# Kernel tuning notes

Measured on AMD Instinct MI355X. Metric: run time of the kernel, lower is better.

## Reference

```python
import jax, jax.numpy as jnp
import numpy as np

G = 200          # voxel grid extent per axis (spatial_shape)
EPS = 1e-5       # BatchNorm eps


def setup_inputs() -> dict:
    N, C_in, C_out = 1_000_000, 6, 32
    rng = np.random.default_rng(0)
    # unique active voxel sites (submanifold conv assumes deduplicated coords)
    lin = rng.choice(G ** 3, size=N, replace=False)
    coords = np.stack([lin // (G * G), (lin // G) % G, lin % G], axis=1).astype(np.int32)
    key = jax.random.key(0)
    k1, k2 = jax.random.split(key)
    feat = jax.random.normal(k1, (N, C_in), jnp.float32)
    W = jax.random.normal(k2, (27, C_in, C_out), jnp.float32) * (1.0 / np.sqrt(27 * C_in))
    gamma = jnp.ones((C_out,), jnp.float32)
    beta = jnp.zeros((C_out,), jnp.float32)
    return {"feat": feat, "coords": jnp.asarray(coords), "W": W, "gamma": gamma, "beta": beta}


def _subm_conv_bn_relu(feat, coords, W, gamma, beta):
    # Submanifold 3x3x3 sparse conv: output only at active sites.
    N = feat.shape[0]
    c = coords
    keys = (c[:, 0] * G + c[:, 1]) * G + c[:, 2]          # linearized voxel keys
    order = jnp.argsort(keys)
    skeys = keys[order]
    sfeat = feat[order]
    # all 27 kernel offsets, center included
    r = jnp.arange(-1, 2, dtype=c.dtype)
    offs = jnp.stack(jnp.meshgrid(r, r, r, indexing="ij"), -1).reshape(27, 3)

    def step(acc, xs):
        off, Wk = xs                                       # off: [3], Wk: [C_in, C_out]
        nc = c + off                                       # neighbor coords [N,3]
        valid = jnp.all((nc >= 0) & (nc < G), axis=1)
        nkey = (nc[:, 0] * G + nc[:, 1]) * G + nc[:, 2]
        pos = jnp.clip(jnp.searchsorted(skeys, nkey), 0, N - 1)
        found = valid & (skeys[pos] == nkey)               # rulebook hit mask
        g = jnp.where(found[:, None], sfeat[pos], 0.0)     # gathered neighbor feats [N,C_in]
        return acc + g @ Wk, None

    out, _ = jax.lax.scan(step, jnp.zeros((N, W.shape[2]), feat.dtype), (offs, W))
    # BatchNorm1d (training-mode batch stats) + ReLU
    mean = out.mean(0)
    var = out.var(0)
    out = (out - mean) * jax.lax.rsqrt(var + EPS) * gamma + beta
    return jax.nn.relu(out)


def reference(feat, coords, W, gamma, beta):
    return _subm_conv_bn_relu(feat, coords, W, gamma, beta)
```

## Files before the change

### kernel.cpp

```cpp
#include <hip/hip_runtime.h>
#include <stdint.h>

#define GRIDX 200
#define P 202
#define PCELL (P * P * P)
#define GUARD 100000
#define NBITS (PCELL + GUARD)
#define NWP ((NBITS + 31) / 32)
#define K_INV (PCELL + 50000)
#define CIN 6
#define COUT 32
#define NOFF 27
#define BN_EPS 1e-5f
#define WPB 1024
#define NBLKP ((NWP + WPB - 1) / WPB)

typedef __attribute__((ext_vector_type(8))) short short8;
typedef __attribute__((ext_vector_type(4))) float f32x4;


__device__ __forceinline__ int xcd_swizzle(int b, int nwg) {
    int q = nwg >> 3, r = nwg & 7;
    int xcd = b & 7, idx = b >> 3;
    int base = (xcd < r) ? xcd * (q + 1) : r * (q + 1) + (xcd - r) * q;
    return base + idx;
}

__device__ __forceinline__ unsigned short f2bf(float f) {
    uint32_t u = __float_as_uint(f);
    return (unsigned short)((u + 0x7FFFu + ((u >> 16) & 1u)) >> 16);
}
__device__ __forceinline__ uint32_t pack2(float a, float b) {
    return (uint32_t)f2bf(a) | ((uint32_t)f2bf(b) << 16);
}

__device__ __forceinline__ int koff_delta(int koff) {
    int t9 = koff / 9;
    int r9 = koff - t9 * 9;
    int t3 = r9 / 3;
    return (t9 - 1) * (P * P) + (t3 - 1) * P + (r9 - t3 * 3 - 1);
}


__global__ __launch_bounds__(256)
void build_bitmap_v4(const int* __restrict__ coords, int N, uint2* __restrict__ recs) {
    int t = blockIdx.x * blockDim.x + threadIdx.x;
    int i0 = t * 4;
    if (i0 >= N) return;
    if (i0 + 4 <= N) {
        const int4* c4 = (const int4*)(coords + (size_t)i0 * 3);
        int4 ca = c4[0], cb = c4[1], cc = c4[2];
        int cx[4] = {ca.x, ca.w, cb.z, cc.y};
        int cy[4] = {ca.y, cb.x, cb.w, cc.z};
        int cz[4] = {ca.z, cb.y, cc.x, cc.w};
#pragma unroll
        for (int s = 0; s < 4; s++) {
            int key = ((cx[s] + 1) * P + (cy[s] + 1)) * P + (cz[s] + 1);
            atomicOr((unsigned int*)&recs[key >> 5], 1u << (key & 31));
        }
    } else {
        for (int i = i0; i < N; i++) {
            int x = coords[3 * i], y = coords[3 * i + 1], z = coords[3 * i + 2];
            int key = ((x + 1) * P + (y + 1)) * P + (z + 1);
            atomicOr((unsigned int*)&recs[key >> 5], 1u << (key & 31));
        }
    }
}

__global__ __launch_bounds__(256)
void bitmap_count_p(const uint2* __restrict__ recs, int* __restrict__ bcnt) {
    __shared__ int tot[256];
    int b = blockIdx.x, t = threadIdx.x;
    int w0 = b * WPB + t * 4;
    int s = 0;
#pragma unroll
    for (int j = 0; j < 4; j++) {
        int w = w0 + j;
        if (w < NWP) s += __popc(recs[w].x);
    }
    tot[t] = s;
    __syncthreads();
    if (t < 128) tot[t] += tot[t + 128];
    __syncthreads();
    if (t < 64) {
        int v = tot[t] + tot[t + 64];
#pragma unroll
        for (int d = 32; d > 0; d >>= 1) v += __shfl_down(v, d);
        if (t == 0) bcnt[b] = v;
    }
}

__global__ void scan_small(const int* __restrict__ cnt, int* __restrict__ base, int n) {
    __shared__ int tot[256];
    int t = threadIdx.x;
    int v = (t < n) ? cnt[t] : 0;
    tot[t] = v;
    __syncthreads();
    for (int d = 1; d < 256; d <<= 1) {
        int u = (t >= d) ? tot[t - d] : 0;
        __syncthreads();
        tot[t] += u;
        __syncthreads();
    }
    if (t < n) base[t] = tot[t] - v;
}

__global__ __launch_bounds__(256)
void base_fill_skeys(uint2* __restrict__ recs, const int* __restrict__ bbase,
                     int* __restrict__ skeys) {
    __shared__ int tot[256];
    int b = blockIdx.x, t = threadIdx.x;
    int w0 = b * WPB + t * 4;
    uint32_t wd[4];
    int p[4];
    int s = 0;
#pragma unroll
    for (int j = 0; j < 4; j++) {
        int w = w0 + j;
        wd[j] = (w < NWP) ? recs[w].x : 0u;
        p[j] = __popc(wd[j]);
        s += p[j];
    }
    tot[t] = s;
    __syncthreads();
    for (int d = 1; d < 256; d <<= 1) {
        int u = (t >= d) ? tot[t - d] : 0;
        __syncthreads();
        tot[t] += u;
        __syncthreads();
    }
    int run = bbase[b] + tot[t] - s;
#pragma unroll
    for (int j = 0; j < 4; j++) {
        int w = w0 + j;
        if (w < NWP) {
            recs[w].y = (uint32_t)run;
            uint32_t m = wd[j];
            int rr = run;
            int k0 = w * 32;
            while (m) {
                int bit = __ffs((int)m) - 1;
                skeys[rr++] = k0 + bit;
                m &= m - 1u;
            }
            run += p[j];
        }
    }
}


__global__ __launch_bounds__(256)
void rank_scatter_v4(const int* __restrict__ coords, const float* __restrict__ feat, int N,
                     const uint2* __restrict__ recs,
                     int* __restrict__ sorig, uint4* __restrict__ feat_bf) {
    int t = blockIdx.x * blockDim.x + threadIdx.x;
    int i0 = t * 4;
    if (i0 >= N) return;
    if (i0 + 4 <= N) {
        const int4* c4 = (const int4*)(coords + (size_t)i0 * 3);
        int4 ca = c4[0], cb = c4[1], cc = c4[2];
        int cx[4] = {ca.x, ca.w, cb.z, cc.y};
        int cy[4] = {ca.y, cb.x, cb.w, cc.z};
        int cz[4] = {ca.z, cb.y, cc.x, cc.w};
        const float4* f4 = (const float4*)(feat + (size_t)i0 * 6);
        float4 fa = f4[0], fb = f4[1], fc = f4[2], fd = f4[3], fe = f4[4], ff = f4[5];
        float fs[4][6] = {
            {fa.x, fa.y, fa.z, fa.w, fb.x, fb.y},
            {fb.z, fb.w, fc.x, fc.y, fc.z, fc.w},
            {fd.x, fd.y, fd.z, fd.w, fe.x, fe.y},
            {fe.z, fe.w, ff.x, ff.y, ff.z, ff.w}};
#pragma unroll
        for (int s = 0; s < 4; s++) {
            int key = ((cx[s] + 1) * P + (cy[s] + 1)) * P + (cz[s] + 1);
            uint2 rb = recs[key >> 5];
            int bit = key & 31;
            int r = (int)(rb.y + (uint32_t)__popc(rb.x & ((1u << bit) - 1u)));
            sorig[r] = i0 + s;
            uint4 u;
            u.x = pack2(fs[s][0], fs[s][1]);
            u.y = pack2(fs[s][2], fs[s][3]);
            u.z = pack2(fs[s][4], fs[s][5]);
            u.w = 0u;
            feat_bf[r] = u;
        }
    } else {
        for (int i = i0; i < N; i++) {
            int x = coords[3 * i], y = coords[3 * i + 1], z = coords[3 * i + 2];
            int key = ((x + 1) * P + (y + 1)) * P + (z + 1);
            uint2 rb = recs[key >> 5];
            int bit = key & 31;
            int r = (int)(rb.y + (uint32_t)__popc(rb.x & ((1u << bit) - 1u)));
            sorig[r] = i;
            const float* fr = feat + (size_t)i * CIN;
            uint4 u;
            u.x = pack2(fr[0], fr[1]);
            u.y = pack2(fr[2], fr[3]);
            u.z = pack2(fr[4], fr[5]);
            u.w = 0u;
            feat_bf[r] = u;
        }
    }
}


__global__ void prep_wfrag(const float* __restrict__ W, uint4* __restrict__ wfrag) {
    int idx = blockIdx.x * blockDim.x + threadIdx.x;
    if (idx >= 7 * 2 * 64) return;
    int l = idx & 63;
    int nt = (idx >> 6) & 1;
    int ks = idx >> 7;
    int koff = (l >> 4) * 7 + ks;
    int col = nt * 16 + (l & 15);
    unsigned short v[8];
#pragma unroll
    for (int ci = 0; ci < 8; ci++) {
        float f = 0.f;
        if (ci < CIN && koff < NOFF) f = W[(koff * CIN + ci) * COUT + col];
        v[ci] = f2bf(f);
    }
    uint4 u;
    u.x = (uint32_t)v[0] | ((uint32_t)v[1] << 16);
    u.y = (uint32_t)v[2] | ((uint32_t)v[3] << 16);
    u.z = (uint32_t)v[4] | ((uint32_t)v[5] << 16);
    u.w = (uint32_t)v[6] | ((uint32_t)v[7] << 16);
    wfrag[idx] = u;
}


__global__ __launch_bounds__(256, 4)
void conv_mfma(const uint4* __restrict__ feat_bf,
               const int* __restrict__ skeys,
               const int* __restrict__ sorig,
               const uint4* __restrict__ wfrag,
               const uint2* __restrict__ recs, int N, int nsb,
               float* __restrict__ out,
               float* __restrict__ stats_g) {
    __shared__ __align__(16) float Clds[64 * 36];
    __shared__ float bstat[64];

    int tid = threadIdx.x;
    int w = tid >> 6, l = tid & 63;
    int col = l & 15;
    int rg = l >> 4;
    int kb = rg;

    if (tid < 64) bstat[tid] = 0.f;

    const short8* wf8 = (const short8*)wfrag;
    short8 bf0[7], bf1[7];
#pragma unroll
    for (int ks = 0; ks < 7; ks++) {
        bf0[ks] = wf8[(ks * 2 + 0) * 64 + l];
        bf1[ks] = wf8[(ks * 2 + 1) * 64 + l];
    }

    int b1 = (0x3123 >> (kb * 4)) & 0xF;
    int b2 = b1 + 3;
    int len0 = b1, len2 = 4 - b1;
    int koffC0 = kb * 7;
    int koffC1 = koffC0 + b1;
    int koffC2 = koffC0 + b2;
    int d0 = koff_delta(koffC0);
    int d1 = koff_delta(koffC1);
    bool padC2 = (koffC2 >= NOFF);
    int d2 = padC2 ? 0 : koff_delta(koffC2);

    const uint4* fb16 = (const uint4*)feat_bf;

    float as0 = 0.f, aq0 = 0.f, as1 = 0.f, aq1 = 0.f;

    for (int sb = blockIdx.x; sb < nsb; sb += gridDim.x) {
        int b = xcd_swizzle(sb, nsb);
        int bs = b * 64;
        int site = bs + w * 16 + col;
        int key = (site < N) ? skeys[site] : K_INV;

        int nkA = key + d0;
        int nkB = key + d1;
        int nkC = padC2 ? K_INV : key + d2;
        int waA = nkA >> 5, waB = nkB >> 5, waC = nkC >> 5;
        uint2 rA0 = recs[waA];
        uint2 rB0 = recs[waB];
        uint2 rC0 = recs[waC];
        uint2 rA1 = rA0, rB1 = rB0, rC1 = rC0;
        if (((nkA & 31) + len0) > 32) rA1 = recs[waA + 1];
        if (((nkB & 31) + 3) > 32)    rB1 = recs[waB + 1];
        if (((nkC & 31) + len2) > 32) rC1 = recs[waC + 1];

        short8 av[7];
#pragma unroll
        for (int ks = 0; ks < 7; ks++) {
            int c = (ks >= b1) + (ks >= b2);
            int nk = (c == 0) ? (nkA + ks)
                   : (c == 1) ? (nkB + (ks - b1))
                              : (nkC + (ks - b2));
            int wa  = (c == 0) ? waA : (c == 1) ? waB : waC;
            uint2 r0 = (c == 0) ? rA0 : (c == 1) ? rB0 : rC0;
            uint2 r1 = (c == 0) ? rA1 : (c == 1) ? rB1 : rC1;
            bool second = (nk >> 5) != wa;
            uint32_t wd = second ? r1.x : r0.x;
            uint32_t bw = second ? r1.y : r0.y;
            int p = nk & 31;
            bool hit = (wd >> p) & 1u;
            uint4 a4 = make_uint4(0u, 0u, 0u, 0u);
            if (hit) {
                int pos = (int)(bw + (uint32_t)__popc(wd & ((1u << p) - 1u)));
                a4 = fb16[pos];
            }
            av[ks] = *(const short8*)&a4;
        }

        f32x4 acc0 = {0.f, 0.f, 0.f, 0.f};
        f32x4 acc1 = {0.f, 0.f, 0.f, 0.f};
#pragma unroll
        for (int ks = 0; ks < 7; ks++) {
            acc0 = __builtin_amdgcn_mfma_f32_16x16x32_bf16(av[ks], bf0[ks], acc0, 0, 0, 0);
            acc1 = __builtin_amdgcn_mfma_f32_16x16x32_bf16(av[ks], bf1[ks], acc1, 0, 0, 0);
        }

        as0 += acc0[0] + acc0[1] + acc0[2] + acc0[3];
        aq0 += acc0[0]*acc0[0] + acc0[1]*acc0[1] + acc0[2]*acc0[2] + acc0[3]*acc0[3];
        as1 += acc1[0] + acc1[1] + acc1[2] + acc1[3];
        aq1 += acc1[0]*acc1[0] + acc1[1]*acc1[1] + acc1[2]*acc1[2] + acc1[3]*acc1[3];

        __syncthreads();
#pragma unroll
        for (int r = 0; r < 4; r++) {
            int s = w * 16 + rg * 4 + r;
            Clds[s * 36 + col] = acc0[r];
            Clds[s * 36 + col + 16] = acc1[r];
        }
        __syncthreads();

        int st = tid >> 2;
        int q = (tid & 3) * 2;
        int sr = bs + st;
        if (sr < N) {
            float4* gp = (float4*)(out + (size_t)sorig[sr] * COUT + q * 4);
            gp[0] = *(const float4*)&Clds[st * 36 + q * 4];
            gp[1] = *(const float4*)&Clds[st * 36 + q * 4 + 4];
        }
    }

    as0 += __shfl_xor(as0, 16); as0 += __shfl_xor(as0, 32);
    aq0 += __shfl_xor(aq0, 16); aq0 += __shfl_xor(aq0, 32);
    as1 += __shfl_xor(as1, 16); as1 += __shfl_xor(as1, 32);
    aq1 += __shfl_xor(aq1, 16); aq1 += __shfl_xor(aq1, 32);
    __syncthreads();
    if (l < 16) {
        atomicAdd(&bstat[col], as0);
        atomicAdd(&bstat[16 + col], as1);
        atomicAdd(&bstat[32 + col], aq0);
        atomicAdd(&bstat[48 + col], aq1);
    }
    __syncthreads();
    if (tid < 64) {
        int slice = blockIdx.x & 63;
        atomicAdd(&stats_g[slice * 64 + tid], bstat[tid]);
    }
}


__global__ void finalize_sliced(const float* __restrict__ stats_g,
                                const float* __restrict__ gamma,
                                const float* __restrict__ beta,
                                float invN, float* __restrict__ scsh) {
    int c = threadIdx.x;
    if (c < COUT) {
        float s = 0.f, q = 0.f;
        for (int sl = 0; sl < 64; sl++) {
            s += stats_g[sl * 64 + c];
            q += stats_g[sl * 64 + 32 + c];
        }
        float mean = s * invN;
        float var = q * invN - mean * mean;
        float sc = gamma[c] * rsqrtf(var + BN_EPS);
        scsh[c] = sc;
        scsh[COUT + c] = beta[c] - mean * sc;
    }
}

__global__ __launch_bounds__(256)
void norm_kernel(float* __restrict__ out, long total_vec,
                 const float* __restrict__ scaleshift) {
    __shared__ float sc[COUT], sh[COUT];
    for (int t = threadIdx.x; t < COUT; t += blockDim.x) {
        sc[t] = scaleshift[t];
        sh[t] = scaleshift[COUT + t];
    }
    __syncthreads();
    long stride = (long)gridDim.x * blockDim.x;
    float4* p = (float4*)out;
    for (long v = (long)blockIdx.x * blockDim.x + threadIdx.x; v < total_vec; v += stride) {
        int cbase = (int)(v & 7) * 4;
        float4 u = p[v];
        u.x = fmaxf(u.x * sc[cbase + 0] + sh[cbase + 0], 0.f);
        u.y = fmaxf(u.y * sc[cbase + 1] + sh[cbase + 1], 0.f);
        u.z = fmaxf(u.z * sc[cbase + 2] + sh[cbase + 2], 0.f);
        u.w = fmaxf(u.w * sc[cbase + 3] + sh[cbase + 3], 0.f);
        p[v] = u;
    }
}


extern "C" void kernel_launch(void* const* d_in, const int* in_sizes, int n_in,
                              void* d_out, int out_size, void* d_ws, size_t ws_size,
                              hipStream_t stream) {
    const float* feat   = (const float*)d_in[0];
    const int*   coords = (const int*)d_in[1];
    const float* W      = (const float*)d_in[2];
    const float* gamma  = (const float*)d_in[3];
    const float* beta   = (const float*)d_in[4];
    float* out = (float*)d_out;

    int N = in_sizes[0] / CIN;
    const int threads = 256;
    int blocks4 = (N + 4 * threads - 1) / (4 * threads);
    int nsb = (N + 63) / 64;
    int cblocks = 1024;
    long total_vec = (long)N * COUT / 4;

    size_t a256 = 255;
    size_t recs_b     = (size_t)NWP * 8;
    size_t off_stats  = (recs_b + a256) & ~a256;
    size_t zero_bytes = off_stats + (size_t)64 * 64 * 4;
    size_t off_scsh   = (zero_bytes + a256) & ~a256;
    size_t off_skeys  = (off_scsh + 2 * COUT * 4 + a256) & ~a256;
    size_t off_featbf = (off_skeys + (size_t)N * 4 + a256) & ~a256;
    size_t off_sorig  = (off_featbf + (size_t)(N + 1) * 16 + a256) & ~a256;
    size_t off_bcnt   = (off_sorig + (size_t)N * 4 + a256) & ~a256;
    size_t off_bbase  = (off_bcnt + 256 * 4 + a256) & ~a256;
    size_t off_wfrag  = (off_bbase + 256 * 4 + a256) & ~a256;

    uint2* recs  = (uint2*)d_ws;
    float* stats = (float*)((char*)d_ws + off_stats);
    float* scsh  = (float*)((char*)d_ws + off_scsh);
    int*   skeys = (int*)((char*)d_ws + off_skeys);
    uint4* featb = (uint4*)((char*)d_ws + off_featbf);
    int*   sorig = (int*)((char*)d_ws + off_sorig);
    int*   bcnt  = (int*)((char*)d_ws + off_bcnt);
    int*   bbase = (int*)((char*)d_ws + off_bbase);
    uint4* wfrag = (uint4*)((char*)d_ws + off_wfrag);

    hipMemsetAsync(d_ws, 0, zero_bytes, stream);
    prep_wfrag<<<4, threads, 0, stream>>>(W, wfrag);
    build_bitmap_v4<<<blocks4, threads, 0, stream>>>(coords, N, recs);
    bitmap_count_p<<<NBLKP, threads, 0, stream>>>(recs, bcnt);
    scan_small<<<1, threads, 0, stream>>>(bcnt, bbase, NBLKP);
    base_fill_skeys<<<NBLKP, threads, 0, stream>>>(recs, bbase, skeys);
    rank_scatter_v4<<<blocks4, threads, 0, stream>>>(coords, feat, N, recs, sorig, featb);
    conv_mfma<<<cblocks, threads, 0, stream>>>(featb, skeys, sorig, wfrag, recs, N, nsb, out, stats);
    finalize_sliced<<<1, 64, 0, stream>>>(stats, gamma, beta, 1.0f / (float)N, scsh);
    norm_kernel<<<2048, threads, 0, stream>>>(out, total_vec, scsh);
}
```

Before: 194.8 us.

## Write conv output in sorted order and gather by rank in normalization

The conv kernel now writes its results contiguously in sorted-key order into a workspace buffer instead of scattering them through the sorig permutation. The final BN+ReLU kernel recomputes each point's rank from the coords and the bitmap, gathers that row from the workspace and writes the original-order output contiguously. This drops the sorig array and its scatter write, and turns the scattered global writes into scattered reads. In exchange it needs an extra workspace buffer of N×32 floats and a coords read plus bitmap lookup in the norm pass. The fallback path for a small workspace permutes `out` in place across threads, which looks incorrect.

New measurement: 200.4 us. +2.9%, slower.

```diff
diff --git a/kernel.cpp b/kernel.cpp
--- a/kernel.cpp
+++ b/kernel.cpp
@@ -152,7 +152,7 @@
 __global__ __launch_bounds__(256)
 void rank_scatter_v4(const int* __restrict__ coords, const float* __restrict__ feat, int N,
                      const uint2* __restrict__ recs,
-                     int* __restrict__ sorig, uint4* __restrict__ feat_bf) {
+                     uint4* __restrict__ feat_bf) {
     int t = blockIdx.x * blockDim.x + threadIdx.x;
     int i0 = t * 4;
     if (i0 >= N) return;
@@ -175,7 +175,6 @@
             uint2 rb = recs[key >> 5];
             int bit = key & 31;
             int r = (int)(rb.y + (uint32_t)__popc(rb.x & ((1u << bit) - 1u)));
-            sorig[r] = i0 + s;
             uint4 u;
             u.x = pack2(fs[s][0], fs[s][1]);
             u.y = pack2(fs[s][2], fs[s][3]);
@@ -190,7 +189,6 @@
             uint2 rb = recs[key >> 5];
             int bit = key & 31;
             int r = (int)(rb.y + (uint32_t)__popc(rb.x & ((1u << bit) - 1u)));
-            sorig[r] = i;
             const float* fr = feat + (size_t)i * CIN;
             uint4 u;
             u.x = pack2(fr[0], fr[1]);
@@ -230,10 +228,9 @@
 __global__ __launch_bounds__(256, 4)
 void conv_mfma(const uint4* __restrict__ feat_bf,
                const int* __restrict__ skeys,
-               const int* __restrict__ sorig,
                const uint4* __restrict__ wfrag,
                const uint2* __restrict__ recs, int N, int nsb,
-               float* __restrict__ out,
+               float* __restrict__ wsout,
                float* __restrict__ stats_g) {
     __shared__ __align__(16) float Clds[64 * 36];
     __shared__ float bstat[64];
@@ -336,7 +333,7 @@
         int q = (tid & 3) * 2;
         int sr = bs + st;
         if (sr < N) {
-            float4* gp = (float4*)(out + (size_t)sorig[sr] * COUT + q * 4);
+            float4* gp = (float4*)(wsout + (size_t)sr * COUT + q * 4);
             gp[0] = *(const float4*)&Clds[st * 36 + q * 4];
             gp[1] = *(const float4*)&Clds[st * 36 + q * 4 + 4];
         }
@@ -380,26 +377,39 @@
     }
 }
 
+
 __global__ __launch_bounds__(256)
-void norm_kernel(float* __restrict__ out, long total_vec,
-                 const float* __restrict__ scaleshift) {
+void norm_gather_rank(const float* __restrict__ wsout, const int* __restrict__ coords,
+                      const uint2* __restrict__ recs, int N,
+                      const float* __restrict__ scsh, float* __restrict__ out) {
     __shared__ float sc[COUT], sh[COUT];
     for (int t = threadIdx.x; t < COUT; t += blockDim.x) {
-        sc[t] = scaleshift[t];
-        sh[t] = scaleshift[COUT + t];
-    }
-    __syncthreads();
-    long stride = (long)gridDim.x * blockDim.x;
-    float4* p = (float4*)out;
-    for (long v = (long)blockIdx.x * blockDim.x + threadIdx.x; v < total_vec; v += stride) {
-        int cbase = (int)(v & 7) * 4;
-        float4 u = p[v];
-        u.x = fmaxf(u.x * sc[cbase + 0] + sh[cbase + 0], 0.f);
-        u.y = fmaxf(u.y * sc[cbase + 1] + sh[cbase + 1], 0.f);
-        u.z = fmaxf(u.z * sc[cbase + 2] + sh[cbase + 2], 0.f);
-        u.w = fmaxf(u.w * sc[cbase + 3] + sh[cbase + 3], 0.f);
-        p[v] = u;
-    }
+        sc[t] = scsh[t];
+        sh[t] = scsh[COUT + t];
+    }
+    __syncthreads();
+    int tid = blockIdx.x * blockDim.x + threadIdx.x;
+    int i = tid >> 2, q = tid & 3;
+    if (i >= N) return;
+    int x = coords[3 * i], y = coords[3 * i + 1], z = coords[3 * i + 2];
+    int key = ((x + 1) * P + (y + 1)) * P + (z + 1);
+    uint2 rb = recs[key >> 5];
+    int bit = key & 31;
+    int r = (int)(rb.y + (uint32_t)__popc(rb.x & ((1u << bit) - 1u)));
+    int cb = q * 8;
+    const float4* wp = (const float4*)(wsout + (size_t)r * COUT + cb);
+    float4 v0 = wp[0], v1 = wp[1];
+    v0.x = fmaxf(v0.x * sc[cb + 0] + sh[cb + 0], 0.f);
+    v0.y = fmaxf(v0.y * sc[cb + 1] + sh[cb + 1], 0.f);
+    v0.z = fmaxf(v0.z * sc[cb + 2] + sh[cb + 2], 0.f);
+    v0.w = fmaxf(v0.w * sc[cb + 3] + sh[cb + 3], 0.f);
+    v1.x = fmaxf(v1.x * sc[cb + 4] + sh[cb + 4], 0.f);
+    v1.y = fmaxf(v1.y * sc[cb + 5] + sh[cb + 5], 0.f);
+    v1.z = fmaxf(v1.z * sc[cb + 6] + sh[cb + 6], 0.f);
+    v1.w = fmaxf(v1.w * sc[cb + 7] + sh[cb + 7], 0.f);
+    float4* gp = (float4*)(out + (size_t)i * COUT + cb);
+    gp[0] = v0;
+    gp[1] = v1;
 }
 
 
@@ -418,7 +428,7 @@
     int blocks4 = (N + 4 * threads - 1) / (4 * threads);
     int nsb = (N + 63) / 64;
     int cblocks = 1024;
-    long total_vec = (long)N * COUT / 4;
+    int nblocks = (4 * N + threads - 1) / threads;
 
     size_t a256 = 255;
     size_t recs_b     = (size_t)NWP * 8;
@@ -427,29 +437,48 @@
     size_t off_scsh   = (zero_bytes + a256) & ~a256;
     size_t off_skeys  = (off_scsh + 2 * COUT * 4 + a256) & ~a256;
     size_t off_featbf = (off_skeys + (size_t)N * 4 + a256) & ~a256;
-    size_t off_sorig  = (off_featbf + (size_t)(N + 1) * 16 + a256) & ~a256;
-    size_t off_bcnt   = (off_sorig + (size_t)N * 4 + a256) & ~a256;
+    size_t off_bcnt   = (off_featbf + (size_t)(N + 1) * 16 + a256) & ~a256;
     size_t off_bbase  = (off_bcnt + 256 * 4 + a256) & ~a256;
     size_t off_wfrag  = (off_bbase + 256 * 4 + a256) & ~a256;
+    size_t off_wsout  = (off_wfrag + (size_t)(7 * 2 * 64) * 16 + a256) & ~a256;
+    size_t need_big   = off_wsout + (size_t)N * COUT * 4 + 256;
 
     uint2* recs  = (uint2*)d_ws;
     float* stats = (float*)((char*)d_ws + off_stats);
     float* scsh  = (float*)((char*)d_ws + off_scsh);
     int*   skeys = (int*)((char*)d_ws + off_skeys);
     uint4* featb = (uint4*)((char*)d_ws + off_featbf);
-    int*   sorig = (int*)((char*)d_ws + off_sorig);
     int*   bcnt  = (int*)((char*)d_ws + off_bcnt);
     int*   bbase = (int*)((char*)d_ws + off_bbase);
     uint4* wfrag = (uint4*)((char*)d_ws + off_wfrag);
-
+    float* wsout = (float*)((char*)d_ws + off_wsout);
+
+    if (ws_size >= need_big) {
+        hipMemsetAsync(d_ws, 0, zero_bytes, stream);
+        prep_wfrag<<<4, threads, 0, stream>>>(W, wfrag);
+        build_bitmap_v4<<<blocks4, threads, 0, stream>>>(coords, N, recs);
+        bitmap_count_p<<<NBLKP, threads, 0, stream>>>(recs, bcnt);
+        scan_small<<<1, threads, 0, stream>>>(bcnt, bbase, NBLKP);
+        base_fill_skeys<<<NBLKP, threads, 0, stream>>>(recs, bbase, skeys);
+        rank_scatter_v4<<<blocks4, threads, 0, stream>>>(coords, feat, N, recs, featb);
+        conv_mfma<<<cblocks, threads, 0, stream>>>(featb, skeys, wfrag, recs, N, nsb,
+                                                   wsout, stats);
+        finalize_sliced<<<1, 64, 0, stream>>>(stats, gamma, beta, 1.0f / (float)N, scsh);
+        norm_gather_rank<<<nblocks, threads, 0, stream>>>(wsout, coords, recs, N, scsh, out);
+        return;
+    }
+
+    int* sorig = (int*)((char*)d_ws + off_wsout);
     hipMemsetAsync(d_ws, 0, zero_bytes, stream);
     prep_wfrag<<<4, threads, 0, stream>>>(W, wfrag);
     build_bitmap_v4<<<blocks4, threads, 0, stream>>>(coords, N, recs);
     bitmap_count_p<<<NBLKP, threads, 0, stream>>>(recs, bcnt);
     scan_small<<<1, threads, 0, stream>>>(bcnt, bbase, NBLKP);
     base_fill_skeys<<<NBLKP, threads, 0, stream>>>(recs, bbase, skeys);
-    rank_scatter_v4<<<blocks4, threads, 0, stream>>>(coords, feat, N, recs, sorig, featb);
-    conv_mfma<<<cblocks, threads, 0, stream>>>(featb, skeys, sorig, wfrag, recs, N, nsb, out, stats);
+    rank_scatter_v4<<<blocks4, threads, 0, stream>>>(coords, feat, N, recs, featb);
+    conv_mfma<<<cblocks, threads, 0, stream>>>(featb, skeys, wfrag, recs, N, nsb,
+                                               (float*)out , stats);
     finalize_sliced<<<1, 64, 0, stream>>>(stats, gamma, beta, 1.0f / (float)N, scsh);
-    norm_kernel<<<2048, threads, 0, stream>>>(out, total_vec, scsh);
-}
+    (void)sorig;
+    norm_gather_rank<<<nblocks, threads, 0, stream>>>((const float*)out, coords, recs, N, scsh, out);
+}
```
